# Kernel optimization log

Hardware: AMD Instinct MI355X
Metric: run time of the kernel (lower is better)

Reference implementation:

```python
import jax, jax.numpy as jnp
import numpy as np

N_NODES = 50000
N_EDGES = 250000
D_IN, D_HID, D_OUT = 768, 256, 2


def _sage_conv(x, src, dst, W_l, b_l, W_r, n_nodes):
    # PyG SAGEConv (aggr='mean', root_weight=True):
    #   out[i] = lin_l(mean_{j in N(i)} x[j]) + lin_r(x[i])
    msg = x[src]  # [E, d] gather of source-node features
    agg = jax.ops.segment_sum(msg, dst, num_segments=n_nodes)
    cnt = jax.ops.segment_sum(jnp.ones((src.shape[0],), x.dtype), dst,
                              num_segments=n_nodes)
    agg = agg / jnp.maximum(cnt, 1.0)[:, None]
    return agg @ W_l.T + b_l + x @ W_r.T


def setup_inputs() -> dict:
    key = jax.random.key(0)
    ks = jax.random.split(key, 7)
    x = jax.random.normal(ks[0], (N_NODES, D_IN), dtype=jnp.float32)
    edge_index = jax.random.randint(ks[1], (2, N_EDGES), 0, N_NODES,
                                    dtype=jnp.int64)
    s1 = 1.0 / np.sqrt(D_IN)
    s2 = 1.0 / np.sqrt(D_HID)
    W1_l = jax.random.uniform(ks[2], (D_HID, D_IN), jnp.float32, -s1, s1)
    W1_r = jax.random.uniform(ks[3], (D_HID, D_IN), jnp.float32, -s1, s1)
    b1 = jnp.zeros((D_HID,), jnp.float32)
    W2_l = jax.random.uniform(ks[4], (D_OUT, D_HID), jnp.float32, -s2, s2)
    W2_r = jax.random.uniform(ks[5], (D_OUT, D_HID), jnp.float32, -s2, s2)
    b2 = jnp.zeros((D_OUT,), jnp.float32)
    return {"x": x, "edge_index": edge_index,
            "W1_l": W1_l, "b1": b1, "W1_r": W1_r,
            "W2_l": W2_l, "b2": b2, "W2_r": W2_r}


def reference(x, edge_index, W1_l, b1, W1_r, W2_l, b2, W2_r):
    src, dst = edge_index[0], edge_index[1]
    n = x.shape[0]
    h = _sage_conv(x, src, dst, W1_l, b1, W1_r, n)
    h = jax.nn.relu(h)
    # dropout is identity in eval mode (deterministic reference)
    out = _sage_conv(h, src, dst, W2_l, b2, W2_r, n)
    return out
```

## Files before the change

kernel.cpp:

```cpp
#include <hip/hip_runtime.h>
#include <stdint.h>


#define D_IN  768
#define D_HID 256
#define N1    512
#define KITERS (D_IN / 32)

typedef __attribute__((ext_vector_type(8))) short short8;
typedef __attribute__((ext_vector_type(4))) float f32x4;

__device__ __forceinline__ void async_copy16(const void* g, void* l) {
  __builtin_amdgcn_global_load_lds(
      (const __attribute__((address_space(1))) unsigned int*)g,
      (__attribute__((address_space(3))) unsigned int*)l,
      16, 0, 0);
}

__device__ __forceinline__ unsigned short f2bf(float f) {
  union { float f; unsigned u; } v; v.f = f;
  unsigned r = v.u + 0x7FFFu + ((v.u >> 16) & 1u);
  return (unsigned short)(r >> 16);
}

__device__ __forceinline__ float bf2f(unsigned short b) {
  union { unsigned u; float f; } v; v.u = ((unsigned)b) << 16;
  return v.f;
}


__global__ void cvtidx_k(const void* __restrict__ eidx,
                         int* __restrict__ src32, int* __restrict__ dst32,
                         int* __restrict__ counts, int E) {
  __shared__ int flag32;
  int tid = threadIdx.x;
  int i = blockIdx.x * 256 + tid;
  unsigned v = (i < E) ? ((const unsigned int*)eidx)[2 * (size_t)i + 1] : 0u;
  unsigned long long any = __ballot(v != 0u);
  if (tid == 0) flag32 = 0;
  __syncthreads();
  if ((tid & 63) == 0 && any) flag32 = 1;
  __syncthreads();
  if (i >= E) return;
  int s, d;
  if (flag32) {
    const int* p = (const int*)eidx;
    s = p[i]; d = p[E + i];
  } else {
    const long long* p = (const long long*)eidx;
    s = (int)p[i]; d = (int)p[E + i];
  }
  src32[i] = s;
  dst32[i] = d;
  atomicAdd(&counts[d], 1);
}

__global__ void scanA_k(const int* __restrict__ counts,
                        int* __restrict__ blockSums, int M) {
  __shared__ int ts[256];
  int b = blockIdx.x, t = threadIdx.x;
  int base = b * 1024 + t * 4;
  int s = 0;
#pragma unroll
  for (int k = 0; k < 4; k++) { int i = base + k; if (i < M) s += counts[i]; }
  ts[t] = s;
  __syncthreads();
  for (int off = 128; off > 0; off >>= 1) {
    if (t < off) ts[t] += ts[t + off];
    __syncthreads();
  }
  if (t == 0) blockSums[b] = ts[0];
}

__global__ void scanC_k(const int* __restrict__ counts,
                        const int* __restrict__ bsums,
                        int* __restrict__ offs, int* __restrict__ cursor,
                        int M, int E, int nb) {
  __shared__ int ts[256];
  __shared__ int bofs;
  int b = blockIdx.x, t = threadIdx.x;
  if (t < 64) {
    int v = (t < nb) ? bsums[t] : 0;
    int orig = v;
#pragma unroll
    for (int off = 1; off < 64; off <<= 1) {
      int u = __shfl_up(v, off);
      if (t >= off) v += u;
    }
    if (t == b) bofs = v - orig;
  }
  int base = b * 1024 + t * 4;
  int v[4]; int s = 0;
#pragma unroll
  for (int k = 0; k < 4; k++) {
    int i = base + k;
    v[k] = (i < M) ? counts[i] : 0;
    s += v[k];
  }
  ts[t] = s;
  __syncthreads();
  for (int off = 1; off < 256; off <<= 1) {
    int x = (t >= off) ? ts[t - off] : 0;
    __syncthreads();
    ts[t] += x;
    __syncthreads();
  }
  int run = bofs + ts[t] - s;
#pragma unroll
  for (int k = 0; k < 4; k++) {
    int i = base + k;
    if (i < M) { offs[i] = run; cursor[i] = run; run += v[k]; }
  }
  if (b == 0 && t == 0) offs[M] = E;
}

__global__ void fill_k(const int* __restrict__ src, const int* __restrict__ dst,
                       int* __restrict__ cursor, int* __restrict__ csr, int E) {
  int i = blockIdx.x * 256 + threadIdx.x;
  if (i >= E) return;
  int pos = atomicAdd(&cursor[dst[i]], 1);
  csr[pos] = src[i];
}


__global__ void cvtw_k(const float* __restrict__ W1l, const float* __restrict__ W1r,
                       unsigned short* __restrict__ wb) {
  int idx = blockIdx.x * 256 + threadIdx.x;
  int total = N1 * (D_IN / 8);
  if (idx >= total) return;
  int row = idx / (D_IN / 8);
  int cpos = (idx % (D_IN / 8)) * 8;
  const float* p = (row < D_HID) ? (W1l + (size_t)row * D_IN + cpos)
                                 : (W1r + (size_t)(row - D_HID) * D_IN + cpos);
  float4 f0 = *(const float4*)p;
  float4 f1 = *(const float4*)(p + 4);
  short8 o;
  o[0] = (short)f2bf(f0.x); o[1] = (short)f2bf(f0.y);
  o[2] = (short)f2bf(f0.z); o[3] = (short)f2bf(f0.w);
  o[4] = (short)f2bf(f1.x); o[5] = (short)f2bf(f1.y);
  o[6] = (short)f2bf(f1.z); o[7] = (short)f2bf(f1.w);
  *(short8*)(wb + (size_t)idx * 8) = o;
}

__global__ __launch_bounds__(256) void gemm_k(
    const float* __restrict__ x,
    const unsigned short* __restrict__ wb,
    unsigned short* __restrict__ Cb, int M, int MT, int mtPerXcd) {
  __shared__ unsigned short As[2][128 * 32];
  __shared__ unsigned short Bs[2][128 * 32];

  const int bid = blockIdx.x;
  const int xcd = bid & 7;
  const int j   = bid >> 3;
  const int mt  = xcd * mtPerXcd + (j >> 2);
  if (mt >= MT) return;
  const int m0 = mt * 128;
  const int n0 = (j & 3) * 128;

  const int tid  = threadIdx.x;
  const int lane = tid & 63;
  const int wid  = tid >> 6;
  const int wr = wid >> 1, wc = wid & 1;
  const int l15  = lane & 15;
  const int quad = lane >> 4;

  const int arow0 = tid >> 2, akg = tid & 3;
  const int arow1 = arow0 + 64;
  const int aswz = akg | ((akg & 1) << 2);
  const float* agp0 = x + (size_t)min(m0 + arow0, M - 1) * D_IN + akg * 8;
  const float* agp1 = x + (size_t)min(m0 + arow1, M - 1) * D_IN + akg * 8;
  const int aoff0 = (arow0 >> 4) * 512 + akg * 128 + ((arow0 & 15) ^ aswz) * 8;
  const int aoff1 = (arow1 >> 4) * 512 + akg * 128 + ((arow1 & 15) ^ aswz) * 8;
  const int pquad = quad | ((quad & 1) << 2);

  const int brow = (tid >> 6) * 16 + (tid & 15);
  const int bcg  = (tid >> 4) & 3;
  const unsigned short* bgp0 = wb + (size_t)(n0 + brow) * D_IN + bcg * 8;
  const unsigned short* bgp1 = wb + (size_t)(n0 + brow + 64) * D_IN + bcg * 8;
  const int boff0 = tid * 8;
  const int boff1 = (tid + 256) * 8;

  f32x4 acc[4][4];
#pragma unroll
  for (int r = 0; r < 4; r++)
#pragma unroll
    for (int c = 0; c < 4; c++) acc[r][c] = (f32x4)0.0f;

  float4 a0_0, a0_1, a0_2, a0_3;
  float4 a1_0, a1_1, a1_2, a1_3;

  a0_0 = *(const float4*)(agp0);
  a0_1 = *(const float4*)(agp0 + 4);
  a0_2 = *(const float4*)(agp1);
  a0_3 = *(const float4*)(agp1 + 4);
  async_copy16(bgp0, &Bs[0][boff0]);
  async_copy16(bgp1, &Bs[0][boff1]);
  a1_0 = *(const float4*)(agp0 + 32);
  a1_1 = *(const float4*)(agp0 + 36);
  a1_2 = *(const float4*)(agp1 + 32);
  a1_3 = *(const float4*)(agp1 + 36);

#define GEMM_BODY(P, AR0, AR1, AR2, AR3)                                      \
  {                                                                           \
    short8 o0, o1;                                                            \
    o0[0] = (short)f2bf(AR0.x); o0[1] = (short)f2bf(AR0.y);                   \
    o0[2] = (short)f2bf(AR0.z); o0[3] = (short)f2bf(AR0.w);                   \
    o0[4] = (short)f2bf(AR1.x); o0[5] = (short)f2bf(AR1.y);                   \
    o0[6] = (short)f2bf(AR1.z); o0[7] = (short)f2bf(AR1.w);                   \
    o1[0] = (short)f2bf(AR2.x); o1[1] = (short)f2bf(AR2.y);                   \
    o1[2] = (short)f2bf(AR2.z); o1[3] = (short)f2bf(AR2.w);                   \
    o1[4] = (short)f2bf(AR3.x); o1[5] = (short)f2bf(AR3.y);                   \
    o1[6] = (short)f2bf(AR3.z); o1[7] = (short)f2bf(AR3.w);                   \
    *(short8*)&As[P][aoff0] = o0;                                             \
    *(short8*)&As[P][aoff1] = o1;                                             \
    __syncthreads();                                                          \
    if (kk + 1 < KITERS) {                                                    \
      const int kn = (kk + 1) * 32;                                           \
      async_copy16(bgp0 + kn, &Bs[P ^ 1][boff0]);                             \
      async_copy16(bgp1 + kn, &Bs[P ^ 1][boff1]);                             \
    }                                                                         \
    if (kk + 2 < KITERS) {                                                    \
      const int kp = (kk + 2) * 32;                                           \
      AR0 = *(const float4*)(agp0 + kp);                                      \
      AR1 = *(const float4*)(agp0 + kp + 4);                                  \
      AR2 = *(const float4*)(agp1 + kp);                                      \
      AR3 = *(const float4*)(agp1 + kp + 4);                                  \
    }                                                                         \
    short8 a[4], b[4];                                                        \
    _Pragma("unroll")                                                         \
    for (int r = 0; r < 4; r++)                                               \
      a[r] = *(const short8*)&As[P][(wr * 4 + r) * 512 + quad * 128 +         \
                                    ((l15 ^ pquad)) * 8];                     \
    _Pragma("unroll")                                                         \
    for (int c = 0; c < 4; c++)                                               \
      b[c] = *(const short8*)&Bs[P][(wc * 4 + c) * 512 + quad * 128 +         \
                                    l15 * 8];                                 \
    _Pragma("unroll")                                                         \
    for (int r = 0; r < 4; r++)                                               \
      _Pragma("unroll")                                                       \
      for (int c = 0; c < 4; c++)                                             \
        acc[r][c] =                                                           \
            __builtin_amdgcn_mfma_f32_16x16x32_bf16(a[r], b[c], acc[r][c],    \
                                                    0, 0, 0);                 \
  }

  for (int it = 0; it < KITERS; it += 2) {
    { const int kk = it;     GEMM_BODY(0, a0_0, a0_1, a0_2, a0_3) }
    { const int kk = it + 1; GEMM_BODY(1, a1_0, a1_1, a1_2, a1_3) }
  }
#undef GEMM_BODY

  const int crow0 = m0 + wr * 64;
  const int ccol0 = n0 + wc * 64;
#pragma unroll
  for (int r = 0; r < 4; r++)
#pragma unroll
    for (int c = 0; c < 4; c++) {
      int col = ccol0 + c * 16 + l15;
#pragma unroll
      for (int reg = 0; reg < 4; reg++) {
        int row = crow0 + r * 16 + quad * 4 + reg;
        Cb[(size_t)row * N1 + col] = f2bf(acc[r][c][reg]);
      }
    }
}

__global__ void agg_l2_k(const unsigned short* __restrict__ Cb,
                         const int* __restrict__ offs, const int* __restrict__ csr,
                         const float* __restrict__ b1,
                         const float* __restrict__ W2l, const float* __restrict__ W2r,
                         float4* __restrict__ rs, int M) {
  int tid = threadIdx.x;
  int lane = tid & 63;
  int wid = tid >> 6;
  int i = blockIdx.x * 4 + wid;
  if (i >= M) return;
  int c = lane * 4;
  float4 bv  = *(const float4*)(b1 + c);
  float4 wl0 = *(const float4*)(W2l + c);
  float4 wl1 = *(const float4*)(W2l + D_HID + c);
  float4 wr0 = *(const float4*)(W2r + c);
  float4 wr1 = *(const float4*)(W2r + D_HID + c);
  int s = offs[i], e = offs[i + 1];
  float ax = 0.f, ay = 0.f, az = 0.f, aw = 0.f;
  for (int t = s; t < e; t++) {
    int j = csr[t];
    ushort4 v = *(const ushort4*)(Cb + (size_t)j * N1 + c);
    ax += bf2f(v.x); ay += bf2f(v.y); az += bf2f(v.z); aw += bf2f(v.w);
  }
  float inv = 1.0f / fmaxf((float)(e - s), 1.0f);
  ushort4 q = *(const ushort4*)(Cb + (size_t)i * N1 + D_HID + c);
  float h0 = fmaxf(ax * inv + bv.x + bf2f(q.x), 0.0f);
  float h1 = fmaxf(ay * inv + bv.y + bf2f(q.y), 0.0f);
  float h2 = fmaxf(az * inv + bv.z + bf2f(q.z), 0.0f);
  float h3 = fmaxf(aw * inv + bv.w + bf2f(q.w), 0.0f);
  float r0 = h0 * wl0.x + h1 * wl0.y + h2 * wl0.z + h3 * wl0.w;
  float r1 = h0 * wl1.x + h1 * wl1.y + h2 * wl1.z + h3 * wl1.w;
  float s0 = h0 * wr0.x + h1 * wr0.y + h2 * wr0.z + h3 * wr0.w;
  float s1 = h0 * wr1.x + h1 * wr1.y + h2 * wr1.z + h3 * wr1.w;
#pragma unroll
  for (int off = 32; off > 0; off >>= 1) {
    r0 += __shfl_xor(r0, off);
    r1 += __shfl_xor(r1, off);
    s0 += __shfl_xor(s0, off);
    s1 += __shfl_xor(s1, off);
  }
  if (lane == 0) rs[i] = make_float4(r0, r1, s0, s1);
}

__global__ void final_k(const float4* __restrict__ rs, const int* __restrict__ offs,
                        const int* __restrict__ csr, const float* __restrict__ b2,
                        float* __restrict__ out, int M) {
  int i = blockIdx.x * 256 + threadIdx.x;
  if (i >= M) return;
  int s = offs[i], e = offs[i + 1];
  float a0 = 0.0f, a1 = 0.0f;
  for (int t = s; t < e; t++) {
    float4 v = rs[csr[t]];
    a0 += v.x; a1 += v.y;
  }
  float inv = 1.0f / fmaxf((float)(e - s), 1.0f);
  float4 me = rs[i];
  out[2 * i + 0] = a0 * inv + b2[0] + me.z;
  out[2 * i + 1] = a1 * inv + b2[1] + me.w;
}


extern "C" void kernel_launch(void* const* d_in, const int* in_sizes, int n_in,
                              void* d_out, int out_size, void* d_ws, size_t ws_size,
                              hipStream_t stream) {
  const float* x   = (const float*)d_in[0];
  const void*  eix = d_in[1];
  const float* W1l = (const float*)d_in[2];
  const float* b1  = (const float*)d_in[3];
  const float* W1r = (const float*)d_in[4];
  const float* W2l = (const float*)d_in[5];
  const float* b2  = (const float*)d_in[6];
  const float* W2r = (const float*)d_in[7];
  float* out = (float*)d_out;

  const int M  = in_sizes[0] / D_IN;
  const int E  = in_sizes[1] / 2;
  const int Mp = ((M + 127) / 128) * 128;
  const int nb = (M + 1023) / 1024;
  const int MT = Mp / 128;
  const int mtPerXcd = (MT + 7) / 8;
  const int gemmBlocks = 8 * mtPerXcd * 4;

  char* ws = (char*)d_ws;
  size_t off = 0;
  auto alloc = [&](size_t b) { size_t o = off; off += (b + 255) & ~(size_t)255; return o; };
  size_t oCounts = alloc((size_t)M * 4);
  size_t zeroBytes = (size_t)M * 4;
  size_t oOffs   = alloc((size_t)(M + 1) * 4);
  size_t oCursor = alloc((size_t)M * 4);
  size_t oCsr    = alloc((size_t)E * 4);
  size_t oSrc    = alloc((size_t)E * 4);
  size_t oDst    = alloc((size_t)E * 4);
  size_t oBSums  = alloc(64 * 4);
  size_t oWb     = alloc((size_t)N1 * D_IN * 2);
  size_t oC      = alloc((size_t)Mp * N1 * 2);
  size_t oRs     = alloc((size_t)M * 16);
  (void)ws_size; (void)n_in; (void)out_size;

  int* counts = (int*)(ws + oCounts);
  int* offs   = (int*)(ws + oOffs);
  int* cursor = (int*)(ws + oCursor);
  int* csr    = (int*)(ws + oCsr);
  int* src32  = (int*)(ws + oSrc);
  int* dst32  = (int*)(ws + oDst);
  int* bsums  = (int*)(ws + oBSums);
  unsigned short* wb = (unsigned short*)(ws + oWb);
  unsigned short* Cb = (unsigned short*)(ws + oC);
  float4* rs = (float4*)(ws + oRs);

  hipMemsetAsync(counts, 0, zeroBytes, stream);

  int gE = (E + 255) / 256;
  cvtidx_k<<<gE, 256, 0, stream>>>(eix, src32, dst32, counts, E);
  scanA_k<<<nb, 256, 0, stream>>>(counts, bsums, M);
  scanC_k<<<nb, 256, 0, stream>>>(counts, bsums, offs, cursor, M, E, nb);
  fill_k<<<gE, 256, 0, stream>>>(src32, dst32, cursor, csr, E);

  int gW = (N1 * (D_IN / 8) + 255) / 256;
  cvtw_k<<<gW, 256, 0, stream>>>(W1l, W1r, wb);

  gemm_k<<<gemmBlocks, 256, 0, stream>>>(x, wb, Cb, M, MT, mtPerXcd);

  agg_l2_k<<<(M + 3) / 4, 256, 0, stream>>>(Cb, offs, csr, b1, W2l, W2r, rs, M);
  final_k<<<(M + 255) / 256, 256, 0, stream>>>(rs, offs, csr, b2, out, M);
}
```

Before: 380.1 us.

## Make GEMM persistent with triple-buffered B and unroll aggregation loops by two

The GEMM becomes a persistent kernel: a fixed grid of 1024 blocks loops over tiles. The B operand is now triple-buffered so its async copies run two K-steps ahead, with an explicit vmcnt wait and a raw barrier in place of __syncthreads. The edge-gather loops in agg_l2_k and final_k are unrolled by two with separate accumulators, which puts more independent loads in flight. In exchange, the hand-tuned waitcnt counts are fragile, the 6-way unroll has to divide KITERS=24 evenly, and the persistent grid can leave some CUs with an uneven share of tiles.

```diff
diff --git a/kernel.cpp b/kernel.cpp
--- a/kernel.cpp
+++ b/kernel.cpp
@@ -142,20 +142,13 @@
   *(short8*)(wb + (size_t)idx * 8) = o;
 }
 
-__global__ __launch_bounds__(256) void gemm_k(
+__global__ __launch_bounds__(256, 4) void gemm_k(
     const float* __restrict__ x,
     const unsigned short* __restrict__ wb,
-    unsigned short* __restrict__ Cb, int M, int MT, int mtPerXcd) {
+    unsigned short* __restrict__ Cb, int M, int MT, int mtPerXcd,
+    int nTiles, int grid) {
   __shared__ unsigned short As[2][128 * 32];
-  __shared__ unsigned short Bs[2][128 * 32];
-
-  const int bid = blockIdx.x;
-  const int xcd = bid & 7;
-  const int j   = bid >> 3;
-  const int mt  = xcd * mtPerXcd + (j >> 2);
-  if (mt >= MT) return;
-  const int m0 = mt * 128;
-  const int n0 = (j & 3) * 128;
+  __shared__ unsigned short Bs[3][128 * 32];
 
   const int tid  = threadIdx.x;
   const int lane = tid & 63;
@@ -167,40 +160,54 @@
   const int arow0 = tid >> 2, akg = tid & 3;
   const int arow1 = arow0 + 64;
   const int aswz = akg | ((akg & 1) << 2);
-  const float* agp0 = x + (size_t)min(m0 + arow0, M - 1) * D_IN + akg * 8;
-  const float* agp1 = x + (size_t)min(m0 + arow1, M - 1) * D_IN + akg * 8;
   const int aoff0 = (arow0 >> 4) * 512 + akg * 128 + ((arow0 & 15) ^ aswz) * 8;
   const int aoff1 = (arow1 >> 4) * 512 + akg * 128 + ((arow1 & 15) ^ aswz) * 8;
   const int pquad = quad | ((quad & 1) << 2);
 
   const int brow = (tid >> 6) * 16 + (tid & 15);
   const int bcg  = (tid >> 4) & 3;
-  const unsigned short* bgp0 = wb + (size_t)(n0 + brow) * D_IN + bcg * 8;
-  const unsigned short* bgp1 = wb + (size_t)(n0 + brow + 64) * D_IN + bcg * 8;
   const int boff0 = tid * 8;
   const int boff1 = (tid + 256) * 8;
 
-  f32x4 acc[4][4];
-#pragma unroll
-  for (int r = 0; r < 4; r++)
-#pragma unroll
-    for (int c = 0; c < 4; c++) acc[r][c] = (f32x4)0.0f;
-
-  float4 a0_0, a0_1, a0_2, a0_3;
-  float4 a1_0, a1_1, a1_2, a1_3;
-
-  a0_0 = *(const float4*)(agp0);
-  a0_1 = *(const float4*)(agp0 + 4);
-  a0_2 = *(const float4*)(agp1);
-  a0_3 = *(const float4*)(agp1 + 4);
-  async_copy16(bgp0, &Bs[0][boff0]);
-  async_copy16(bgp1, &Bs[0][boff1]);
-  a1_0 = *(const float4*)(agp0 + 32);
-  a1_1 = *(const float4*)(agp0 + 36);
-  a1_2 = *(const float4*)(agp1 + 32);
-  a1_3 = *(const float4*)(agp1 + 36);
-
-#define GEMM_BODY(P, AR0, AR1, AR2, AR3)                                      \
+  for (int t = blockIdx.x; t < nTiles; t += grid) {
+    const int xcd = t & 7;
+    const int j   = t >> 3;
+    const int mt  = xcd * mtPerXcd + (j >> 2);
+    if (mt >= MT) continue;
+    const int m0 = mt * 128;
+    const int n0 = (j & 3) * 128;
+
+    const float* agp0 = x + (size_t)min(m0 + arow0, M - 1) * D_IN + akg * 8;
+    const float* agp1 = x + (size_t)min(m0 + arow1, M - 1) * D_IN + akg * 8;
+    const unsigned short* bgp0 = wb + (size_t)(n0 + brow) * D_IN + bcg * 8;
+    const unsigned short* bgp1 = wb + (size_t)(n0 + brow + 64) * D_IN + bcg * 8;
+
+    f32x4 acc[4][4];
+#pragma unroll
+    for (int r = 0; r < 4; r++)
+#pragma unroll
+      for (int c = 0; c < 4; c++) acc[r][c] = (f32x4)0.0f;
+
+    float4 a0_0, a0_1, a0_2, a0_3;
+    float4 a1_0, a1_1, a1_2, a1_3;
+
+    async_copy16(bgp0, &Bs[0][boff0]);
+    async_copy16(bgp1, &Bs[0][boff1]);
+    asm volatile("" ::: "memory");
+    a0_0 = *(const float4*)(agp0);
+    a0_1 = *(const float4*)(agp0 + 4);
+    a0_2 = *(const float4*)(agp1);
+    a0_3 = *(const float4*)(agp1 + 4);
+    asm volatile("" ::: "memory");
+    async_copy16(bgp0 + 32, &Bs[1][boff0]);
+    async_copy16(bgp1 + 32, &Bs[1][boff1]);
+    asm volatile("" ::: "memory");
+    a1_0 = *(const float4*)(agp0 + 32);
+    a1_1 = *(const float4*)(agp0 + 36);
+    a1_2 = *(const float4*)(agp1 + 32);
+    a1_3 = *(const float4*)(agp1 + 36);
+
+#define GEMM_BODY(P, BR, BW, AR0, AR1, AR2, AR3)                              \
   {                                                                           \
     short8 o0, o1;                                                            \
     o0[0] = (short)f2bf(AR0.x); o0[1] = (short)f2bf(AR0.y);                   \
@@ -213,18 +220,18 @@
     o1[6] = (short)f2bf(AR3.z); o1[7] = (short)f2bf(AR3.w);                   \
     *(short8*)&As[P][aoff0] = o0;                                             \
     *(short8*)&As[P][aoff1] = o1;                                             \
-    __syncthreads();                                                          \
-    if (kk + 1 < KITERS) {                                                    \
-      const int kn = (kk + 1) * 32;                                           \
-      async_copy16(bgp0 + kn, &Bs[P ^ 1][boff0]);                             \
-      async_copy16(bgp1 + kn, &Bs[P ^ 1][boff1]);                             \
-    }                                                                         \
+    asm volatile("s_waitcnt vmcnt(6) lgkmcnt(0)" ::: "memory");               \
+    __builtin_amdgcn_s_barrier();                                             \
     if (kk + 2 < KITERS) {                                                    \
-      const int kp = (kk + 2) * 32;                                           \
-      AR0 = *(const float4*)(agp0 + kp);                                      \
-      AR1 = *(const float4*)(agp0 + kp + 4);                                  \
-      AR2 = *(const float4*)(agp1 + kp);                                      \
-      AR3 = *(const float4*)(agp1 + kp + 4);                                  \
+      const int kn = (kk + 2) * 32;                                           \
+      async_copy16(bgp0 + kn, &Bs[BW][boff0]);                                \
+      async_copy16(bgp1 + kn, &Bs[BW][boff1]);                                \
+      asm volatile("" ::: "memory");                                          \
+      AR0 = *(const float4*)(agp0 + kn);                                      \
+      AR1 = *(const float4*)(agp0 + kn + 4);                                  \
+      AR2 = *(const float4*)(agp1 + kn);                                      \
+      AR3 = *(const float4*)(agp1 + kn + 4);                                  \
+      asm volatile("" ::: "memory");                                          \
     }                                                                         \
     short8 a[4], b[4];                                                        \
     _Pragma("unroll")                                                         \
@@ -233,8 +240,8 @@
                                     ((l15 ^ pquad)) * 8];                     \
     _Pragma("unroll")                                                         \
     for (int c = 0; c < 4; c++)                                               \
-      b[c] = *(const short8*)&Bs[P][(wc * 4 + c) * 512 + quad * 128 +         \
-                                    l15 * 8];                                 \
+      b[c] = *(const short8*)&Bs[BR][(wc * 4 + c) * 512 + quad * 128 +        \
+                                     l15 * 8];                                \
     _Pragma("unroll")                                                         \
     for (int r = 0; r < 4; r++)                                               \
       _Pragma("unroll")                                                       \
@@ -244,25 +251,30 @@
                                                     0, 0, 0);                 \
   }
 
-  for (int it = 0; it < KITERS; it += 2) {
-    { const int kk = it;     GEMM_BODY(0, a0_0, a0_1, a0_2, a0_3) }
-    { const int kk = it + 1; GEMM_BODY(1, a1_0, a1_1, a1_2, a1_3) }
-  }
+    for (int it = 0; it < KITERS; it += 6) {
+      { const int kk = it + 0; GEMM_BODY(0, 0, 2, a0_0, a0_1, a0_2, a0_3) }
+      { const int kk = it + 1; GEMM_BODY(1, 1, 0, a1_0, a1_1, a1_2, a1_3) }
+      { const int kk = it + 2; GEMM_BODY(0, 2, 1, a0_0, a0_1, a0_2, a0_3) }
+      { const int kk = it + 3; GEMM_BODY(1, 0, 2, a1_0, a1_1, a1_2, a1_3) }
+      { const int kk = it + 4; GEMM_BODY(0, 1, 0, a0_0, a0_1, a0_2, a0_3) }
+      { const int kk = it + 5; GEMM_BODY(1, 2, 1, a1_0, a1_1, a1_2, a1_3) }
+    }
 #undef GEMM_BODY
 
-  const int crow0 = m0 + wr * 64;
-  const int ccol0 = n0 + wc * 64;
-#pragma unroll
-  for (int r = 0; r < 4; r++)
-#pragma unroll
-    for (int c = 0; c < 4; c++) {
-      int col = ccol0 + c * 16 + l15;
-#pragma unroll
-      for (int reg = 0; reg < 4; reg++) {
-        int row = crow0 + r * 16 + quad * 4 + reg;
-        Cb[(size_t)row * N1 + col] = f2bf(acc[r][c][reg]);
+    const int crow0 = m0 + wr * 64;
+    const int ccol0 = n0 + wc * 64;
+#pragma unroll
+    for (int r = 0; r < 4; r++)
+#pragma unroll
+      for (int c = 0; c < 4; c++) {
+        int col = ccol0 + c * 16 + l15;
+#pragma unroll
+        for (int reg = 0; reg < 4; reg++) {
+          int row = crow0 + r * 16 + quad * 4 + reg;
+          Cb[(size_t)row * N1 + col] = f2bf(acc[r][c][reg]);
+        }
       }
-    }
+  }
 }
 
 __global__ void agg_l2_k(const unsigned short* __restrict__ Cb,
@@ -282,14 +294,25 @@
   float4 wr0 = *(const float4*)(W2r + c);
   float4 wr1 = *(const float4*)(W2r + D_HID + c);
   int s = offs[i], e = offs[i + 1];
+  ushort4 q = *(const ushort4*)(Cb + (size_t)i * N1 + D_HID + c);
   float ax = 0.f, ay = 0.f, az = 0.f, aw = 0.f;
-  for (int t = s; t < e; t++) {
+  float bx = 0.f, by = 0.f, bz = 0.f, bw = 0.f;
+  int t = s;
+  for (; t + 2 <= e; t += 2) {
+    int j0 = csr[t];
+    int j1 = csr[t + 1];
+    ushort4 v0 = *(const ushort4*)(Cb + (size_t)j0 * N1 + c);
+    ushort4 v1 = *(const ushort4*)(Cb + (size_t)j1 * N1 + c);
+    ax += bf2f(v0.x); ay += bf2f(v0.y); az += bf2f(v0.z); aw += bf2f(v0.w);
+    bx += bf2f(v1.x); by += bf2f(v1.y); bz += bf2f(v1.z); bw += bf2f(v1.w);
+  }
+  if (t < e) {
     int j = csr[t];
     ushort4 v = *(const ushort4*)(Cb + (size_t)j * N1 + c);
     ax += bf2f(v.x); ay += bf2f(v.y); az += bf2f(v.z); aw += bf2f(v.w);
   }
+  ax += bx; ay += by; az += bz; aw += bw;
   float inv = 1.0f / fmaxf((float)(e - s), 1.0f);
-  ushort4 q = *(const ushort4*)(Cb + (size_t)i * N1 + D_HID + c);
   float h0 = fmaxf(ax * inv + bv.x + bf2f(q.x), 0.0f);
   float h1 = fmaxf(ay * inv + bv.y + bf2f(q.y), 0.0f);
   float h2 = fmaxf(az * inv + bv.z + bf2f(q.z), 0.0f);
@@ -314,11 +337,16 @@
   int i = blockIdx.x * 256 + threadIdx.x;
   if (i >= M) return;
   int s = offs[i], e = offs[i + 1];
-  float a0 = 0.0f, a1 = 0.0f;
-  for (int t = s; t < e; t++) {
-    float4 v = rs[csr[t]];
-    a0 += v.x; a1 += v.y;
-  }
+  float a0 = 0.0f, a1 = 0.0f, b0 = 0.0f, b1 = 0.0f;
+  int t = s;
+  for (; t + 2 <= e; t += 2) {
+    float4 v0 = rs[csr[t]];
+    float4 v1 = rs[csr[t + 1]];
+    a0 += v0.x; a1 += v0.y;
+    b0 += v1.x; b1 += v1.y;
+  }
+  if (t < e) { float4 v = rs[csr[t]]; a0 += v.x; a1 += v.y; }
+  a0 += b0; a1 += b1;
   float inv = 1.0f / fmaxf((float)(e - s), 1.0f);
   float4 me = rs[i];
   out[2 * i + 0] = a0 * inv + b2[0] + me.z;
@@ -345,7 +373,8 @@
   const int nb = (M + 1023) / 1024;
   const int MT = Mp / 128;
   const int mtPerXcd = (MT + 7) / 8;
-  const int gemmBlocks = 8 * mtPerXcd * 4;
+  const int nTiles = 8 * mtPerXcd * 4;
+  const int gemmGrid = 1024;
 
   char* ws = (char*)d_ws;
   size_t off = 0;
@@ -385,7 +414,8 @@
   int gW = (N1 * (D_IN / 8) + 255) / 256;
   cvtw_k<<<gW, 256, 0, stream>>>(W1l, W1r, wb);
 
-  gemm_k<<<gemmBlocks, 256, 0, stream>>>(x, wb, Cb, M, MT, mtPerXcd);
+  gemm_k<<<gemmGrid, 256, 0, stream>>>(x, wb, Cb, M, MT, mtPerXcd,
+                                       nTiles, gemmGrid);
 
   agg_l2_k<<<(M + 3) / 4, 256, 0, stream>>>(Cb, offs, csr, b1, W2l, W2r, rs, M);
   final_k<<<(M + 255) / 256, 256, 0, stream>>>(rs, offs, csr, b2, out, M);
```

Measured after the change: 493.5 us. 29.9% more time.
